# Kernel tuning notes

Measured on AMD Instinct MI355X. Metric: run time of the kernel, lower is better.

The kernel has to match this reference:

```python
import jax, jax.numpy as jnp
import numpy as np

WIN_SIZE = 11
WIN_SIGMA = 1.5
DATA_RANGE = 255.0
K1, K2 = 0.01, 0.03


def _gauss_win():
    # matches _fspecial_gauss_1d(11, 1.5)
    coords = jnp.arange(WIN_SIZE, dtype=jnp.float32) - WIN_SIZE // 2
    g = jnp.exp(-(coords ** 2) / (2.0 * WIN_SIGMA ** 2))
    return g / g.sum()


def _gaussian_filter(x, win):
    # separable depthwise blur, 'valid' padding (padding=0 in torch), groups=C
    C = x.shape[1]
    dn = ('NCHW', 'OIHW', 'NCHW')
    kh = jnp.tile(win.reshape(1, 1, WIN_SIZE, 1), (C, 1, 1, 1))
    kw = jnp.tile(win.reshape(1, 1, 1, WIN_SIZE), (C, 1, 1, 1))
    out = jax.lax.conv_general_dilated(x, kh, (1, 1), 'VALID',
                                       dimension_numbers=dn, feature_group_count=C)
    out = jax.lax.conv_general_dilated(out, kw, (1, 1), 'VALID',
                                       dimension_numbers=dn, feature_group_count=C)
    return out


def setup_inputs() -> dict:
    key = jax.random.key(0)
    k1, k2 = jax.random.split(key)
    shape = (16, 3, 512, 512)
    X = jax.random.uniform(k1, shape, dtype=jnp.float32) * DATA_RANGE
    Y = jax.random.uniform(k2, shape, dtype=jnp.float32) * DATA_RANGE
    return {'X': X, 'Y': Y}


def reference(X, Y):
    win = _gauss_win()
    C1 = (K1 * DATA_RANGE) ** 2
    C2 = (K2 * DATA_RANGE) ** 2
    mu1 = _gaussian_filter(X, win)
    mu2 = _gaussian_filter(Y, win)
    mu1_sq = mu1 * mu1
    mu2_sq = mu2 * mu2
    mu1_mu2 = mu1 * mu2
    sigma1_sq = _gaussian_filter(X * X, win) - mu1_sq
    sigma2_sq = _gaussian_filter(Y * Y, win) - mu2_sq
    sigma12 = _gaussian_filter(X * Y, win) - mu1_mu2
    cs_map = (2.0 * sigma12 + C2) / (sigma1_sq + sigma2_sq + C2)
    ssim_map = (2.0 * mu1_mu2 + C1) / (mu1_sq + mu2_sq + C1) * cs_map
    # torch: mean over channel dim then squeeze(0) (no-op for N>1)
    ssim_map = jnp.mean(ssim_map, axis=1)  # [N, H-10, W-10]
    return 1.0 - ssim_map
```

## Files before the change

### kernel.cpp

```cpp
#include <hip/hip_runtime.h>


namespace {

constexpr int NN = 16, CC = 3, HH = 512, WW = 512;
constexpr int OH = HH - 10, OW = WW - 10;
constexpr int TW = 64, TH = 32;
constexpr int SROWS = 48, SREAL = 42;
constexpr int SCOLS = 80, SPITCH = 88;
constexpr int HPITCH = 48;
constexpr float C1c = 6.5025f;
constexpr float C2c = 58.5225f;

typedef _Float16 half8   __attribute__((ext_vector_type(8)));
typedef _Float16 half4   __attribute__((ext_vector_type(4)));
typedef float    floatv4 __attribute__((ext_vector_type(4)));

__device__ const float WF[11] = {
    0.00102838f, 0.00759876f, 0.03600077f, 0.10936069f, 0.21300553f,
    0.26601172f,
    0.21300553f, 0.10936069f, 0.03600077f, 0.00759876f, 0.00102838f
};

__global__ __launch_bounds__(256, 4)
void ssim_kernel(const float* __restrict__ X, const float* __restrict__ Y,
                 float* __restrict__ out)
{
    __shared__ __align__(16) _Float16 s_x[SROWS][SPITCH];
    __shared__ __align__(16) _Float16 s_y[SROWS][SPITCH];
    __shared__ __align__(16) _Float16 s_ht[2][TW][HPITCH];
    __shared__ _Float16 s_wtab[16];

    const int tid  = threadIdx.x;
    const int lane = tid & 63;
    const int wv   = tid >> 6;
    const int col0 = blockIdx.x * TW;
    const int row0 = blockIdx.y * TH;
    const int n    = blockIdx.z;

    if (tid < 16) s_wtab[tid] = (tid < 11) ? (_Float16)WF[tid] : (_Float16)0.f;
    {
        const _Float16 z0 = (_Float16)0.f;
        const half4 z4 = {z0, z0, z0, z0};
        for (int i = tid; i < (SROWS - SREAL) * (SCOLS / 4); i += 256) {
            int r = SREAL + i / (SCOLS / 4), c4 = (i % (SCOLS / 4)) * 4;
            *(half4*)&s_x[r][c4] = z4;
            *(half4*)&s_y[r][c4] = z4;
        }
    }
    __syncthreads();

    half8 bfrag;
    {
        const int bn = lane & 15, kq = (lane >> 4) * 8;
        #pragma unroll
        for (int j = 0; j < 8; ++j) {
            int kk = kq + j - bn;
            kk = (kk < 0 || kk > 10) ? 11 : kk;
            bfrag[j] = s_wtab[kk];
        }
    }

    float acc[2][4] = {{0.f,0.f,0.f,0.f},{0.f,0.f,0.f,0.f}};

    const size_t plane = (size_t)HH * WW;
    const float* Xn = X + (size_t)n * CC * plane;
    const float* Yn = Y + (size_t)n * CC * plane;
    const bool fastcol = (col0 + SCOLS <= WW);

    const floatv4 zf = {0.f, 0.f, 0.f, 0.f};
    const int arow = lane & 15;
    const int aq   = lane >> 4;
    const int crow = (lane >> 4) * 4;

    for (int ch = 0; ch < CC; ++ch) {
        const float* Xc = Xn + (size_t)ch * plane;
        const float* Yc = Yn + (size_t)ch * plane;

        if (ch > 0) __syncthreads();

        if (fastcol) {
            for (int i = tid; i < SREAL * (SCOLS / 4); i += 256) {
                int r = i / (SCOLS / 4), c4 = (i % (SCOLS / 4)) * 4;
                int gr = row0 + r; gr = gr < HH ? gr : HH - 1;
                float4 vx = *(const float4*)(Xc + (size_t)gr * WW + col0 + c4);
                float4 vy = *(const float4*)(Yc + (size_t)gr * WW + col0 + c4);
                half4 hx = {(_Float16)vx.x, (_Float16)vx.y,
                            (_Float16)vx.z, (_Float16)vx.w};
                half4 hy = {(_Float16)vy.x, (_Float16)vy.y,
                            (_Float16)vy.z, (_Float16)vy.w};
                *(half4*)&s_x[r][c4] = hx;
                *(half4*)&s_y[r][c4] = hy;
            }
        } else {
            for (int i = tid; i < SREAL * (SCOLS / 4); i += 256) {
                int r = i / (SCOLS / 4), c4 = (i % (SCOLS / 4)) * 4;
                int gr = row0 + r; gr = gr < HH ? gr : HH - 1;
                float ax[4], ay[4];
                #pragma unroll
                for (int e = 0; e < 4; ++e) {
                    int gw = col0 + c4 + e; gw = gw < WW ? gw : WW - 1;
                    ax[e] = Xc[(size_t)gr * WW + gw];
                    ay[e] = Yc[(size_t)gr * WW + gw];
                }
                half4 hx = {(_Float16)ax[0], (_Float16)ax[1],
                            (_Float16)ax[2], (_Float16)ax[3]};
                half4 hy = {(_Float16)ay[0], (_Float16)ay[1],
                            (_Float16)ay[2], (_Float16)ay[3]};
                *(half4*)&s_x[r][c4] = hx;
                *(half4*)&s_y[r][c4] = hy;
            }
        }
        __syncthreads();

        half8 axf[3], ayf[3];
        #pragma unroll
        for (int rc = 0; rc < 3; ++rc) {
            axf[rc] = *(const half8*)&s_x[rc*16 + arow][wv*16 + aq*8];
            ayf[rc] = *(const half8*)&s_y[rc*16 + arow][wv*16 + aq*8];
        }

        floatv4 vfr[5][2];
        #pragma unroll
        for (int q = 0; q < 5; ++q) {
            _Float16* hb = &s_ht[q & 1][0][0];
            #pragma unroll
            for (int rc = 0; rc < 3; ++rc) {
                half8 a;
                if      (q == 0) a = axf[rc];
                else if (q == 1) a = ayf[rc];
                else if (q == 2) a = axf[rc] * axf[rc];
                else if (q == 3) a = ayf[rc] * ayf[rc];
                else             a = axf[rc] * ayf[rc];
                floatv4 d = __builtin_amdgcn_mfma_f32_16x16x32_f16(
                    a, bfrag, zf, 0, 0, 0);
                half4 h = {(_Float16)d[0], (_Float16)d[1],
                           (_Float16)d[2], (_Float16)d[3]};
                *(half4*)&hb[(wv*16 + arow) * HPITCH + rc*16 + crow] = h;
            }
            #pragma unroll
            for (int b = 0; b < 2; ++b) {
                half8 av = *(const half8*)
                    &hb[(wv*16 + arow) * HPITCH + b*16 + aq*8];
                vfr[q][b] = __builtin_amdgcn_mfma_f32_16x16x32_f16(
                    av, bfrag, zf, 0, 0, 0);
            }
        }

        #pragma unroll
        for (int b = 0; b < 2; ++b) {
            #pragma unroll
            for (int p = 0; p < 4; ++p) {
                float m1 = vfr[0][b][p], m2 = vfr[1][b][p];
                float exx = vfr[2][b][p], eyy = vfr[3][b][p],
                      exy = vfr[4][b][p];
                float m1s = m1*m1, m2s = m2*m2, m12 = m1*m2;
                float s1 = exx - m1s, s2 = eyy - m2s, s12 = exy - m12;
                float n1 = 2.f*m12 + C1c, d1 = m1s + m2s + C1c;
                float n2 = 2.f*s12 + C2c, d2 = s1 + s2 + C2c;
                acc[b][p] = fmaf(n1 * n2, __builtin_amdgcn_rcpf(d1 * d2),
                                 acc[b][p]);
            }
        }
    }

    #pragma unroll
    for (int b = 0; b < 2; ++b) {
        const int orow = row0 + b*16 + arow;
        const int ocol = col0 + wv*16 + crow;
        if (orow < OH) {
            float r0v = 1.f - acc[b][0] * (1.f/3.f);
            float r1v = 1.f - acc[b][1] * (1.f/3.f);
            float r2v = 1.f - acc[b][2] * (1.f/3.f);
            float r3v = 1.f - acc[b][3] * (1.f/3.f);
            size_t base = ((size_t)n * OH + orow) * OW + ocol;
            if (ocol + 3 < OW) {
                *(float2*)(out + base)     = make_float2(r0v, r1v);
                *(float2*)(out + base + 2) = make_float2(r2v, r3v);
            } else {
                float rs[4] = {r0v, r1v, r2v, r3v};
                #pragma unroll
                for (int p = 0; p < 4; ++p)
                    if (ocol + p < OW) out[base + p] = rs[p];
            }
        }
    }
}

}

extern "C" void kernel_launch(void* const* d_in, const int* in_sizes, int n_in,
                              void* d_out, int out_size, void* d_ws, size_t ws_size,
                              hipStream_t stream) {
    const float* X = (const float*)d_in[0];
    const float* Y = (const float*)d_in[1];
    float* out = (float*)d_out;

    dim3 grid((OW + TW - 1) / TW,
              (OH + TH - 1) / TH,
              NN);
    ssim_kernel<<<grid, 256, 0, stream>>>(X, Y, out);
}
```

Before: 146.5 us.

## Prefetch next channel's tiles into registers while computing the current channel

Global loads for the next channel are issued into registers right after the current channel's shared-memory fragments are read. The fp16 conversion and shared-memory write happen at the top of the next iteration, so load latency overlaps the MFMA blur work. This costs 32 extra VGPRs for the staged float4 values, which could hurt occupancy under launch_bounds(256,4). It also replaces the per-block fast/slow column path with a per-chunk bounds check.

Result: slower. 189.2 us (+29.1%).

```diff
diff --git a/kernel.cpp b/kernel.cpp
--- a/kernel.cpp
+++ b/kernel.cpp
@@ -8,6 +8,8 @@
 constexpr int TW = 64, TH = 32;
 constexpr int SROWS = 48, SREAL = 42;
 constexpr int SCOLS = 80, SPITCH = 88;
+constexpr int SCHUNKS = SCOLS / 4;
+constexpr int SITEMS  = SREAL * SCHUNKS;
 constexpr int HPITCH = 48;
 constexpr float C1c = 6.5025f;
 constexpr float C2c = 58.5225f;
@@ -42,8 +44,8 @@
     {
         const _Float16 z0 = (_Float16)0.f;
         const half4 z4 = {z0, z0, z0, z0};
-        for (int i = tid; i < (SROWS - SREAL) * (SCOLS / 4); i += 256) {
-            int r = SREAL + i / (SCOLS / 4), c4 = (i % (SCOLS / 4)) * 4;
+        for (int i = tid; i < (SROWS - SREAL) * SCHUNKS; i += 256) {
+            int r = SREAL + i / SCHUNKS, c4 = (i % SCHUNKS) * 4;
             *(half4*)&s_x[r][c4] = z4;
             *(half4*)&s_y[r][c4] = z4;
         }
@@ -66,51 +68,62 @@
     const size_t plane = (size_t)HH * WW;
     const float* Xn = X + (size_t)n * CC * plane;
     const float* Yn = Y + (size_t)n * CC * plane;
-    const bool fastcol = (col0 + SCOLS <= WW);
 
     const floatv4 zf = {0.f, 0.f, 0.f, 0.f};
     const int arow = lane & 15;
     const int aq   = lane >> 4;
     const int crow = (lane >> 4) * 4;
 
-    for (int ch = 0; ch < CC; ++ch) {
+    float4 px[4], py[4];
+
+    auto prefetch = [&](int ch) {
         const float* Xc = Xn + (size_t)ch * plane;
         const float* Yc = Yn + (size_t)ch * plane;
-
-        if (ch > 0) __syncthreads();
-
-        if (fastcol) {
-            for (int i = tid; i < SREAL * (SCOLS / 4); i += 256) {
-                int r = i / (SCOLS / 4), c4 = (i % (SCOLS / 4)) * 4;
+        #pragma unroll
+        for (int r4 = 0; r4 < 4; ++r4) {
+            const int i = tid + r4 * 256;
+            if (i < SITEMS) {
+                int r = i / SCHUNKS, c4 = (i % SCHUNKS) * 4;
                 int gr = row0 + r; gr = gr < HH ? gr : HH - 1;
-                float4 vx = *(const float4*)(Xc + (size_t)gr * WW + col0 + c4);
-                float4 vy = *(const float4*)(Yc + (size_t)gr * WW + col0 + c4);
-                half4 hx = {(_Float16)vx.x, (_Float16)vx.y,
-                            (_Float16)vx.z, (_Float16)vx.w};
-                half4 hy = {(_Float16)vy.x, (_Float16)vy.y,
-                            (_Float16)vy.z, (_Float16)vy.w};
+                const float* bx = Xc + (size_t)gr * WW;
+                const float* by = Yc + (size_t)gr * WW;
+                if (col0 + c4 + 3 < WW) {
+                    px[r4] = *(const float4*)(bx + col0 + c4);
+                    py[r4] = *(const float4*)(by + col0 + c4);
+                } else {
+                    float ax[4], ay[4];
+                    #pragma unroll
+                    for (int e = 0; e < 4; ++e) {
+                        int gw = col0 + c4 + e; gw = gw < WW ? gw : WW - 1;
+                        ax[e] = bx[gw]; ay[e] = by[gw];
+                    }
+                    px[r4] = make_float4(ax[0], ax[1], ax[2], ax[3]);
+                    py[r4] = make_float4(ay[0], ay[1], ay[2], ay[3]);
+                }
+            }
+        }
+    };
+
+    auto write_lds = [&]() {
+        #pragma unroll
+        for (int r4 = 0; r4 < 4; ++r4) {
+            const int i = tid + r4 * 256;
+            if (i < SITEMS) {
+                int r = i / SCHUNKS, c4 = (i % SCHUNKS) * 4;
+                half4 hx = {(_Float16)px[r4].x, (_Float16)px[r4].y,
+                            (_Float16)px[r4].z, (_Float16)px[r4].w};
+                half4 hy = {(_Float16)py[r4].x, (_Float16)py[r4].y,
+                            (_Float16)py[r4].z, (_Float16)py[r4].w};
                 *(half4*)&s_x[r][c4] = hx;
                 *(half4*)&s_y[r][c4] = hy;
             }
-        } else {
-            for (int i = tid; i < SREAL * (SCOLS / 4); i += 256) {
-                int r = i / (SCOLS / 4), c4 = (i % (SCOLS / 4)) * 4;
-                int gr = row0 + r; gr = gr < HH ? gr : HH - 1;
-                float ax[4], ay[4];
-                #pragma unroll
-                for (int e = 0; e < 4; ++e) {
-                    int gw = col0 + c4 + e; gw = gw < WW ? gw : WW - 1;
-                    ax[e] = Xc[(size_t)gr * WW + gw];
-                    ay[e] = Yc[(size_t)gr * WW + gw];
-                }
-                half4 hx = {(_Float16)ax[0], (_Float16)ax[1],
-                            (_Float16)ax[2], (_Float16)ax[3]};
-                half4 hy = {(_Float16)ay[0], (_Float16)ay[1],
-                            (_Float16)ay[2], (_Float16)ay[3]};
-                *(half4*)&s_x[r][c4] = hx;
-                *(half4*)&s_y[r][c4] = hy;
-            }
-        }
+        }
+    };
+
+    prefetch(0);
+
+    for (int ch = 0; ch < CC; ++ch) {
+        write_lds();
         __syncthreads();
 
         half8 axf[3], ayf[3];
@@ -119,6 +132,9 @@
             axf[rc] = *(const half8*)&s_x[rc*16 + arow][wv*16 + aq*8];
             ayf[rc] = *(const half8*)&s_y[rc*16 + arow][wv*16 + aq*8];
         }
+        __syncthreads();
+
+        if (ch + 1 < CC) prefetch(ch + 1);
 
         floatv4 vfr[5][2];
         #pragma unroll
```

## Load MFMA input fragments straight from global memory, dropping shared staging

Applied to the files above, without the earlier changes.

Each lane now reads its own 8-float input fragments for X and Y directly from global memory into registers and packs them to fp16. This removes the shared-memory input tiles, their zero-fill, and the per-channel block barriers. The horizontal-pass scratch buffer drops from double to single buffering, and the launch bound goes from 4 to 2 blocks per SM. The trade-off is redundant global loads, since neighbouring waves' fragments overlap and reads go through cache, plus higher register pressure. Padding rows now hold clamped real pixel values instead of zeros.

Result: faster. 140.4 us (-4.2%).

```diff
diff --git a/kernel.cpp b/kernel.cpp
--- a/kernel.cpp
+++ b/kernel.cpp
@@ -6,8 +6,6 @@
 constexpr int NN = 16, CC = 3, HH = 512, WW = 512;
 constexpr int OH = HH - 10, OW = WW - 10;
 constexpr int TW = 64, TH = 32;
-constexpr int SROWS = 48, SREAL = 42;
-constexpr int SCOLS = 80, SPITCH = 88;
 constexpr int HPITCH = 48;
 constexpr float C1c = 6.5025f;
 constexpr float C2c = 58.5225f;
@@ -22,13 +20,17 @@
     0.21300553f, 0.10936069f, 0.03600077f, 0.00759876f, 0.00102838f
 };
 
-__global__ __launch_bounds__(256, 4)
+__device__ inline half8 pack8(const float4& a, const float4& b) {
+    half8 h = {(_Float16)a.x, (_Float16)a.y, (_Float16)a.z, (_Float16)a.w,
+               (_Float16)b.x, (_Float16)b.y, (_Float16)b.z, (_Float16)b.w};
+    return h;
+}
+
+__global__ __launch_bounds__(256, 2)
 void ssim_kernel(const float* __restrict__ X, const float* __restrict__ Y,
                  float* __restrict__ out)
 {
-    __shared__ __align__(16) _Float16 s_x[SROWS][SPITCH];
-    __shared__ __align__(16) _Float16 s_y[SROWS][SPITCH];
-    __shared__ __align__(16) _Float16 s_ht[2][TW][HPITCH];
+    __shared__ __align__(16) _Float16 s_ht[TW][HPITCH];
     __shared__ _Float16 s_wtab[16];
 
     const int tid  = threadIdx.x;
@@ -39,15 +41,6 @@
     const int n    = blockIdx.z;
 
     if (tid < 16) s_wtab[tid] = (tid < 11) ? (_Float16)WF[tid] : (_Float16)0.f;
-    {
-        const _Float16 z0 = (_Float16)0.f;
-        const half4 z4 = {z0, z0, z0, z0};
-        for (int i = tid; i < (SROWS - SREAL) * (SCOLS / 4); i += 256) {
-            int r = SREAL + i / (SCOLS / 4), c4 = (i % (SCOLS / 4)) * 4;
-            *(half4*)&s_x[r][c4] = z4;
-            *(half4*)&s_y[r][c4] = z4;
-        }
-    }
     __syncthreads();
 
     half8 bfrag;
@@ -61,69 +54,51 @@
         }
     }
 
+    const int arow = lane & 15;
+    const int aq   = lane >> 4;
+    const int crow = aq * 4;
+
+    int gcol = col0 + wv * 16 + aq * 8;
+    gcol = gcol <= WW - 8 ? gcol : WW - 8;
+    int grow[3];
+    #pragma unroll
+    for (int rc = 0; rc < 3; ++rc) {
+        int g = row0 + rc * 16 + arow;
+        grow[rc] = g < HH ? g : HH - 1;
+    }
+
     float acc[2][4] = {{0.f,0.f,0.f,0.f},{0.f,0.f,0.f,0.f}};
 
     const size_t plane = (size_t)HH * WW;
     const float* Xn = X + (size_t)n * CC * plane;
     const float* Yn = Y + (size_t)n * CC * plane;
-    const bool fastcol = (col0 + SCOLS <= WW);
-
     const floatv4 zf = {0.f, 0.f, 0.f, 0.f};
-    const int arow = lane & 15;
-    const int aq   = lane >> 4;
-    const int crow = (lane >> 4) * 4;
 
     for (int ch = 0; ch < CC; ++ch) {
         const float* Xc = Xn + (size_t)ch * plane;
         const float* Yc = Yn + (size_t)ch * plane;
 
-        if (ch > 0) __syncthreads();
-
-        if (fastcol) {
-            for (int i = tid; i < SREAL * (SCOLS / 4); i += 256) {
-                int r = i / (SCOLS / 4), c4 = (i % (SCOLS / 4)) * 4;
-                int gr = row0 + r; gr = gr < HH ? gr : HH - 1;
-                float4 vx = *(const float4*)(Xc + (size_t)gr * WW + col0 + c4);
-                float4 vy = *(const float4*)(Yc + (size_t)gr * WW + col0 + c4);
-                half4 hx = {(_Float16)vx.x, (_Float16)vx.y,
-                            (_Float16)vx.z, (_Float16)vx.w};
-                half4 hy = {(_Float16)vy.x, (_Float16)vy.y,
-                            (_Float16)vy.z, (_Float16)vy.w};
-                *(half4*)&s_x[r][c4] = hx;
-                *(half4*)&s_y[r][c4] = hy;
-            }
-        } else {
-            for (int i = tid; i < SREAL * (SCOLS / 4); i += 256) {
-                int r = i / (SCOLS / 4), c4 = (i % (SCOLS / 4)) * 4;
-                int gr = row0 + r; gr = gr < HH ? gr : HH - 1;
-                float ax[4], ay[4];
-                #pragma unroll
-                for (int e = 0; e < 4; ++e) {
-                    int gw = col0 + c4 + e; gw = gw < WW ? gw : WW - 1;
-                    ax[e] = Xc[(size_t)gr * WW + gw];
-                    ay[e] = Yc[(size_t)gr * WW + gw];
-                }
-                half4 hx = {(_Float16)ax[0], (_Float16)ax[1],
-                            (_Float16)ax[2], (_Float16)ax[3]};
-                half4 hy = {(_Float16)ay[0], (_Float16)ay[1],
-                            (_Float16)ay[2], (_Float16)ay[3]};
-                *(half4*)&s_x[r][c4] = hx;
-                *(half4*)&s_y[r][c4] = hy;
-            }
+        float4 fx[3][2], fy[3][2];
+        #pragma unroll
+        for (int rc = 0; rc < 3; ++rc) {
+            const float* bx = Xc + (size_t)grow[rc] * WW + gcol;
+            const float* by = Yc + (size_t)grow[rc] * WW + gcol;
+            fx[rc][0] = *(const float4*)bx;
+            fx[rc][1] = *(const float4*)(bx + 4);
+            fy[rc][0] = *(const float4*)by;
+            fy[rc][1] = *(const float4*)(by + 4);
         }
-        __syncthreads();
 
         half8 axf[3], ayf[3];
         #pragma unroll
         for (int rc = 0; rc < 3; ++rc) {
-            axf[rc] = *(const half8*)&s_x[rc*16 + arow][wv*16 + aq*8];
-            ayf[rc] = *(const half8*)&s_y[rc*16 + arow][wv*16 + aq*8];
+            axf[rc] = pack8(fx[rc][0], fx[rc][1]);
+            ayf[rc] = pack8(fy[rc][0], fy[rc][1]);
         }
 
         floatv4 vfr[5][2];
         #pragma unroll
         for (int q = 0; q < 5; ++q) {
-            _Float16* hb = &s_ht[q & 1][0][0];
             #pragma unroll
             for (int rc = 0; rc < 3; ++rc) {
                 half8 a;
@@ -136,12 +111,11 @@
                     a, bfrag, zf, 0, 0, 0);
                 half4 h = {(_Float16)d[0], (_Float16)d[1],
                            (_Float16)d[2], (_Float16)d[3]};
-                *(half4*)&hb[(wv*16 + arow) * HPITCH + rc*16 + crow] = h;
+                *(half4*)&s_ht[wv*16 + arow][rc*16 + crow] = h;
             }
             #pragma unroll
             for (int b = 0; b < 2; ++b) {
-                half8 av = *(const half8*)
-                    &hb[(wv*16 + arow) * HPITCH + b*16 + aq*8];
+                half8 av = *(const half8*)&s_ht[wv*16 + arow][b*16 + aq*8];
                 vfr[q][b] = __builtin_amdgcn_mfma_f32_16x16x32_f16(
                     av, bfrag, zf, 0, 0, 0);
             }
```
